# Kernel tuning notes

Measured on AMD Instinct MI355X. Metric: run time of the kernel, lower is better.

The kernel has to match this reference:

```python
import jax, jax.numpy as jnp
import numpy as np

EPS = 0.05
THRESH = 1e-6
MAX_ITER = 100


def _l2norm(x):
    # matches torch F.normalize(dim=-1): x / max(||x||, 1e-12)
    n = jnp.sqrt(jnp.sum(x * x, axis=-1, keepdims=True))
    return x / jnp.maximum(n, 1e-12)


def setup_inputs() -> dict:
    key = jax.random.key(0)
    kq, kk, kv = jax.random.split(key, 3)
    B, N, D = 8, 1024, 64
    return {
        "q": jax.random.normal(kq, (B, N, D), dtype=jnp.float32),
        "k": jax.random.normal(kk, (B, N, D), dtype=jnp.float32),
        "V": jax.random.normal(kv, (B, N, D), dtype=jnp.float32),
    }


def reference(q, k, V):
    B, N, D = q.shape
    Q = _l2norm(q)
    Kn = _l2norm(k)
    # cost matrix: 1 - cosine similarity, shape (B, N, N)
    C = 1.0 - jnp.einsum("bnd,bmd->bnm", Q, Kn)

    log_mu = jnp.full((B, N), jnp.log(1.0 / N + 1e-8), dtype=C.dtype)
    log_nu = log_mu

    def kernel(u, v):
        # (-C + u_i + v_j) / eps, shape (B, N, N)
        return (-C + u[:, :, None] + v[:, None, :]) / EPS

    def step(carry, _):
        u, v, done = carry
        u0 = u
        u_new = EPS * (log_mu - jax.scipy.special.logsumexp(kernel(u, v), axis=2)) + u
        v_new = EPS * (log_nu - jax.scipy.special.logsumexp(kernel(u_new, v), axis=1)) + v
        err = jnp.mean(jnp.abs(u_new - u0))
        # replicate torch early-break: once converged, freeze u, v
        u = jnp.where(done, u, u_new)
        v = jnp.where(done, v, v_new)
        done = jnp.logical_or(done, err < THRESH)
        return (u, v, done), None

    u0 = jnp.zeros((B, N), dtype=C.dtype)
    v0 = jnp.zeros((B, N), dtype=C.dtype)
    (u, v, _), _ = jax.lax.scan(
        jax.checkpoint(step), (u0, v0, jnp.array(False)), None, length=MAX_ITER
    )

    T = jnp.exp(kernel(u, v))  # transport plan (B, N, N)
    out = jnp.einsum("bnm,bmd->bnd", T, V) + V
    return out
```

## Files before the change

### kernel.cpp

```cpp
#include <hip/hip_runtime.h>
#include <math.h>

#define BB 8
#define NN 1024
#define DD 64
#define EPSF 0.05f
#define MAX_ITER 100
#define ERR_FX_THRESH 8590u
#define SCALE_ 28.853900817779268f
#define EPSLN2_ 0.034657359027997264f
#define NBLK 256
#define NPER 32

typedef __attribute__((ext_vector_type(8))) short short8;
typedef __attribute__((ext_vector_type(4))) float f32x4;

static __device__ __forceinline__ float fexp2(float x) { return __builtin_amdgcn_exp2f(x); }
static __device__ __forceinline__ float flog2(float x) { return __builtin_amdgcn_logf(x); }
static __device__ __forceinline__ float bflo(unsigned u) { return __uint_as_float(u << 16); }
static __device__ __forceinline__ unsigned short bf16rne(float x) {
    unsigned u = __float_as_uint(x);
    u += 0x7fffu + ((u >> 16) & 1u);
    return (unsigned short)(u >> 16);
}
__device__ __forceinline__ float wave_sum64(float x) {
#pragma unroll
    for (int off = 1; off < 64; off <<= 1) x += __shfl_xor(x, off);
    return x;
}

#define CNT64IDX(p, b) ((b) * 200 + (p))

__global__ __launch_bounds__(256) void norm_kernel(const float* __restrict__ q,
                                                   const float* __restrict__ k,
                                                   unsigned short* __restrict__ Qn,
                                                   unsigned short* __restrict__ Kn) {
    int tid = threadIdx.x;
    int bi = blockIdx.x;
    const float* src = (bi < 128) ? q : k;
    unsigned short* dst = (bi < 128) ? Qn : Kn;
    int row = (bi & 127) * 64 + (tid >> 2);
    int c = tid & 3;
    const float* rp = src + ((size_t)row << 6) + c * 16;
    float4 x0 = ((const float4*)rp)[0];
    float4 x1 = ((const float4*)rp)[1];
    float4 x2 = ((const float4*)rp)[2];
    float4 x3 = ((const float4*)rp)[3];
    float ss = x0.x * x0.x + x0.y * x0.y + x0.z * x0.z + x0.w * x0.w
             + x1.x * x1.x + x1.y * x1.y + x1.z * x1.z + x1.w * x1.w
             + x2.x * x2.x + x2.y * x2.y + x2.z * x2.z + x2.w * x2.w
             + x3.x * x3.x + x3.y * x3.y + x3.z * x3.z + x3.w * x3.w;
    ss += __shfl_xor(ss, 1);
    ss += __shfl_xor(ss, 2);
    float sc = 1.0f / fmaxf(sqrtf(ss), 1e-12f);
    unsigned pk[8];
    pk[0] = (unsigned)bf16rne(x0.x * sc) | ((unsigned)bf16rne(x0.y * sc) << 16);
    pk[1] = (unsigned)bf16rne(x0.z * sc) | ((unsigned)bf16rne(x0.w * sc) << 16);
    pk[2] = (unsigned)bf16rne(x1.x * sc) | ((unsigned)bf16rne(x1.y * sc) << 16);
    pk[3] = (unsigned)bf16rne(x1.z * sc) | ((unsigned)bf16rne(x1.w * sc) << 16);
    pk[4] = (unsigned)bf16rne(x2.x * sc) | ((unsigned)bf16rne(x2.y * sc) << 16);
    pk[5] = (unsigned)bf16rne(x2.z * sc) | ((unsigned)bf16rne(x2.w * sc) << 16);
    pk[6] = (unsigned)bf16rne(x3.x * sc) | ((unsigned)bf16rne(x3.y * sc) << 16);
    pk[7] = (unsigned)bf16rne(x3.z * sc) | ((unsigned)bf16rne(x3.w * sc) << 16);
    unsigned short* op = dst + ((size_t)row << 6) + c * 16;
    ((uint4*)op)[0] = make_uint4(pk[0], pk[1], pk[2], pk[3]);
    ((uint4*)op)[1] = make_uint4(pk[4], pk[5], pk[6], pk[7]);
}

__global__ __launch_bounds__(256) void cost_kernel(const unsigned short* __restrict__ Qn,
                                                   const unsigned short* __restrict__ Kn,
                                                   unsigned short* __restrict__ M,
                                                   unsigned short* __restrict__ MT,
                                                   float* __restrict__ vz) {
    __shared__ __align__(16) unsigned short Qb[64][72];
    __shared__ __align__(16) unsigned short Kb[64][72];
    __shared__ __align__(16) unsigned short Ms[64][72];
    __shared__ __align__(16) unsigned short MsT[64][72];
    int b = blockIdx.z;
    int i0 = blockIdx.y * 64, j0 = blockIdx.x * 64;
    int tid = threadIdx.x;
    if (blockIdx.x == 0 && blockIdx.y == 0 && blockIdx.z == 0) {
        float4 z4 = {0.f, 0.f, 0.f, 0.f};
        for (int i = tid; i < 2848; i += 256) ((float4*)vz)[i] = z4;
    }
#pragma unroll
    for (int s = 0; s < 2; ++s) {
        int idx = tid + 256 * s;
        int row = idx >> 3, seg = idx & 7;
        *(uint4*)&Qb[row][seg * 8] =
            *(const uint4*)(Qn + (((size_t)b * NN + i0 + row) << 6) + seg * 8);
        *(uint4*)&Kb[row][seg * 8] =
            *(const uint4*)(Kn + (((size_t)b * NN + j0 + row) << 6) + seg * 8);
    }
    __syncthreads();
    int w = tid >> 6, lane = tid & 63;
    int m = lane & 15, qq = lane >> 4;
    int rloc = w * 16;
    short8 a0 = *(const short8*)&Qb[rloc + m][qq * 8];
    short8 a1 = *(const short8*)&Qb[rloc + m][qq * 8 + 32];
    f32x4 acc[4];
#pragma unroll
    for (int nt = 0; nt < 4; ++nt) {
        short8 b0 = *(const short8*)&Kb[nt * 16 + m][qq * 8];
        short8 b1 = *(const short8*)&Kb[nt * 16 + m][qq * 8 + 32];
        f32x4 z = {0.f, 0.f, 0.f, 0.f};
        z = __builtin_amdgcn_mfma_f32_16x16x32_bf16(a0, b0, z, 0, 0, 0);
        acc[nt] = __builtin_amdgcn_mfma_f32_16x16x32_bf16(a1, b1, z, 0, 0, 0);
    }
#pragma unroll
    for (int nt = 0; nt < 4; ++nt) {
        unsigned short us[4];
#pragma unroll
        for (int r = 0; r < 4; ++r)
            us[r] = bf16rne(fexp2((acc[nt][r] - 1.0f) * SCALE_));
#pragma unroll
        for (int r = 0; r < 4; ++r)
            Ms[rloc + qq * 4 + r][nt * 16 + m] = us[r];
        uint2 t;
        t.x = (unsigned)us[0] | ((unsigned)us[1] << 16);
        t.y = (unsigned)us[2] | ((unsigned)us[3] << 16);
        *(uint2*)&MsT[nt * 16 + m][rloc + qq * 4] = t;
    }
    __syncthreads();
#pragma unroll
    for (int s = 0; s < 2; ++s) {
        int idx = tid + 256 * s;
        int row = idx >> 3, seg = idx & 7;
        *(uint4*)(M + ((size_t)b << 20) + ((size_t)(i0 + row) << 10) + j0 + seg * 8) =
            *(const uint4*)&Ms[row][seg * 8];
        *(uint4*)(MT + ((size_t)b << 20) + ((size_t)(j0 + row) << 10) + i0 + seg * 8) =
            *(const uint4*)&MsT[row][seg * 8];
    }
}

#define ACC8(U4, base)                                              \
    s0 = fmaf(bflo(U4.x), wrg[base + 0], s0);                       \
    s1 = fmaf(__uint_as_float(U4.x), wrg[base + 1], s1);            \
    s0 = fmaf(bflo(U4.y), wrg[base + 2], s0);                       \
    s1 = fmaf(__uint_as_float(U4.y), wrg[base + 3], s1);            \
    s0 = fmaf(bflo(U4.z), wrg[base + 4], s0);                       \
    s1 = fmaf(__uint_as_float(U4.z), wrg[base + 5], s1);            \
    s0 = fmaf(bflo(U4.w), wrg[base + 6], s0);                       \
    s1 = fmaf(__uint_as_float(U4.w), wrg[base + 7], s1);

__global__ __launch_bounds__(256, 1) void sink_coop(const unsigned short* __restrict__ M,
                                                    const unsigned short* MT,
                                                    float* __restrict__ u,
                                                    float* __restrict__ v,
                                                    unsigned long long* __restrict__ cnt64,
                                                    const float* __restrict__ V,
                                                    unsigned short* WT,
                                                    float eln) {
    __shared__ __align__(16) float sw[1280];
    __shared__ float sdel[4];
    __shared__ int sflag;
    int tid = threadIdx.x;
    int w = tid >> 6, lane = tid & 63;
    int b = blockIdx.x & 7;
    int slice = blockIdx.x >> 3;
    int rbase = slice * 32 + w * 8;
    const unsigned short* Mb  = M  + ((size_t)b << 20);
    const unsigned short* MTb = MT + ((size_t)b << 20);
    float* ub = u + (b << 10);
    float* vb = v + (b << 10);

    uint4 mA[8], mB[8], nA[8], nB[8];
#pragma unroll
    for (int r = 0; r < 8; ++r) {
        const uint4* rp = (const uint4*)(Mb + ((size_t)(rbase + r) << 10));
        mA[r] = rp[lane * 2];
        mB[r] = rp[lane * 2 + 1];
        const uint4* tp = (const uint4*)(MTb + ((size_t)(rbase + r) << 10));
        nA[r] = tp[lane * 2];
        nB[r] = tp[lane * 2 + 1];
    }

    float uprev[8], vreg[8];
#pragma unroll
    for (int r = 0; r < 8; ++r) { uprev[r] = 0.f; vreg[r] = 0.f; }

    unsigned myerr = 0xffffffffu;

    for (int t = 0; t < MAX_ITER; ++t) {
        {
            float4 ex;
            ex.x = fexp2(__hip_atomic_load(vb + tid * 4 + 0, __ATOMIC_RELAXED, __HIP_MEMORY_SCOPE_AGENT) * SCALE_);
            ex.y = fexp2(__hip_atomic_load(vb + tid * 4 + 1, __ATOMIC_RELAXED, __HIP_MEMORY_SCOPE_AGENT) * SCALE_);
            ex.z = fexp2(__hip_atomic_load(vb + tid * 4 + 2, __ATOMIC_RELAXED, __HIP_MEMORY_SCOPE_AGENT) * SCALE_);
            ex.w = fexp2(__hip_atomic_load(vb + tid * 4 + 3, __ATOMIC_RELAXED, __HIP_MEMORY_SCOPE_AGENT) * SCALE_);
            *(float4*)&sw[tid * 4 + 4 * (tid >> 2)] = ex;
            __syncthreads();
            float wrg[16];
            *(float4*)&wrg[0]  = *(const float4*)&sw[lane * 20 + 0];
            *(float4*)&wrg[4]  = *(const float4*)&sw[lane * 20 + 4];
            *(float4*)&wrg[8]  = *(const float4*)&sw[lane * 20 + 8];
            *(float4*)&wrg[12] = *(const float4*)&sw[lane * 20 + 12];
            float del = 0.f;
#pragma unroll
            for (int rr = 0; rr < 8; ++rr) {
                float s0 = 0.f, s1 = 0.f;
                ACC8(mA[rr], 0)
                ACC8(mB[rr], 8)
                float s = wave_sum64(s0 + s1);
                float un = eln - EPSLN2_ * flog2(s);
                del += fabsf(un - uprev[rr]);
                uprev[rr] = un;
                if (lane == 0)
                    __hip_atomic_store(ub + rbase + rr, un, __ATOMIC_RELAXED, __HIP_MEMORY_SCOPE_AGENT);
            }
            if (lane == 0) sdel[w] = del;
            asm volatile("s_waitcnt vmcnt(0)" ::: "memory");
            __syncthreads();
            if (tid == 0) {
                float dsum = sdel[0] + sdel[1] + sdel[2] + sdel[3];
                unsigned dfx = (unsigned)fminf(dsum * 1048576.0f, 6.0e7f) + 1u;
                unsigned long long* c = cnt64 + CNT64IDX(2 * t, b);
                unsigned long long tot =
                    __hip_atomic_fetch_add(c, (1ULL << 32) | (unsigned long long)dfx,
                                           __ATOMIC_RELAXED, __HIP_MEMORY_SCOPE_AGENT) +
                    ((1ULL << 32) | (unsigned long long)dfx);
                while ((unsigned)(tot >> 32) < NPER) {
                    __builtin_amdgcn_s_sleep(1);
                    tot = __hip_atomic_load(c, __ATOMIC_RELAXED, __HIP_MEMORY_SCOPE_AGENT);
                }
                myerr = (unsigned)tot;
            }
            __syncthreads();
        }
        {
            float4 ex;
            ex.x = fexp2(__hip_atomic_load(ub + tid * 4 + 0, __ATOMIC_RELAXED, __HIP_MEMORY_SCOPE_AGENT) * SCALE_);
            ex.y = fexp2(__hip_atomic_load(ub + tid * 4 + 1, __ATOMIC_RELAXED, __HIP_MEMORY_SCOPE_AGENT) * SCALE_);
            ex.z = fexp2(__hip_atomic_load(ub + tid * 4 + 2, __ATOMIC_RELAXED, __HIP_MEMORY_SCOPE_AGENT) * SCALE_);
            ex.w = fexp2(__hip_atomic_load(ub + tid * 4 + 3, __ATOMIC_RELAXED, __HIP_MEMORY_SCOPE_AGENT) * SCALE_);
            *(float4*)&sw[tid * 4 + 4 * (tid >> 2)] = ex;
            __syncthreads();
            float wrg[16];
            *(float4*)&wrg[0]  = *(const float4*)&sw[lane * 20 + 0];
            *(float4*)&wrg[4]  = *(const float4*)&sw[lane * 20 + 4];
            *(float4*)&wrg[8]  = *(const float4*)&sw[lane * 20 + 8];
            *(float4*)&wrg[12] = *(const float4*)&sw[lane * 20 + 12];
#pragma unroll
            for (int rr = 0; rr < 8; ++rr) {
                float s0 = 0.f, s1 = 0.f;
                ACC8(nA[rr], 0)
                ACC8(nB[rr], 8)
                float s = wave_sum64(s0 + s1);
                float vn = eln - EPSLN2_ * flog2(s);
                vreg[rr] = vn;
                if (lane == 0)
                    __hip_atomic_store(vb + rbase + rr, vn, __ATOMIC_RELAXED, __HIP_MEMORY_SCOPE_AGENT);
            }
            asm volatile("s_waitcnt vmcnt(0)" ::: "memory");
            __syncthreads();
            if (tid == 0) {
                unsigned long long* c = cnt64 + CNT64IDX(2 * t + 1, b);
                unsigned long long tot =
                    __hip_atomic_fetch_add(c, 1ULL << 32, __ATOMIC_RELAXED, __HIP_MEMORY_SCOPE_AGENT) +
                    (1ULL << 32);
                while ((unsigned)(tot >> 32) < NPER) {
                    __builtin_amdgcn_s_sleep(1);
                    tot = __hip_atomic_load(c, __ATOMIC_RELAXED, __HIP_MEMORY_SCOPE_AGENT);
                }
                int brk = 0;
                if (myerr < ERR_FX_THRESH) {
                    unsigned long long s = 0;
                    for (int bb = 0; bb < 8; ++bb) {
                        unsigned long long tv = __hip_atomic_load(cnt64 + CNT64IDX(2 * t, bb),
                                                                  __ATOMIC_RELAXED, __HIP_MEMORY_SCOPE_AGENT);
                        while ((unsigned)(tv >> 32) < NPER) {
                            __builtin_amdgcn_s_sleep(1);
                            tv = __hip_atomic_load(cnt64 + CNT64IDX(2 * t, bb),
                                                   __ATOMIC_RELAXED, __HIP_MEMORY_SCOPE_AGENT);
                        }
                        s += (unsigned long long)(unsigned)tv;
                    }
                    brk = (s < (unsigned long long)ERR_FX_THRESH);
                }
                sflag = brk;
            }
            __syncthreads();
            if (sflag) break;
        }
    }

    {
        __syncthreads();
        float* swj = &sw[1152];
        unsigned short* T = (unsigned short*)sw;
#pragma unroll
        for (int r = 0; r < 8; ++r)
            if (lane == r) swj[w * 8 + r] = fexp2(vreg[r] * SCALE_);
        __syncthreads();
        int jr = lane >> 3;
        int seg = lane & 7;
        int j = rbase + jr;
        float wj = swj[w * 8 + jr];
        const float* Vp = V + ((((size_t)(b << 10)) + j) << 6) + seg * 8;
        float4 x0 = *(const float4*)(Vp);
        float4 x1 = *(const float4*)(Vp + 4);
        int jloc = w * 8 + jr;
        int d0 = seg * 8;
        T[(d0 + 0) * 36 + jloc] = bf16rne(x0.x * wj);
        T[(d0 + 1) * 36 + jloc] = bf16rne(x0.y * wj);
        T[(d0 + 2) * 36 + jloc] = bf16rne(x0.z * wj);
        T[(d0 + 3) * 36 + jloc] = bf16rne(x0.w * wj);
        T[(d0 + 4) * 36 + jloc] = bf16rne(x1.x * wj);
        T[(d0 + 5) * 36 + jloc] = bf16rne(x1.y * wj);
        T[(d0 + 6) * 36 + jloc] = bf16rne(x1.z * wj);
        T[(d0 + 7) * 36 + jloc] = bf16rne(x1.w * wj);
        __syncthreads();
        int d = tid >> 2, q4 = tid & 3;
        const unsigned short* tr = &T[d * 36 + q4 * 8];
        uint4 o;
        o.x = (unsigned)tr[0] | ((unsigned)tr[1] << 16);
        o.y = (unsigned)tr[2] | ((unsigned)tr[3] << 16);
        o.z = (unsigned)tr[4] | ((unsigned)tr[5] << 16);
        o.w = (unsigned)tr[6] | ((unsigned)tr[7] << 16);
        *(uint4*)(WT + ((size_t)b << 16) + ((size_t)d << 10) + slice * 32 + q4 * 8) = o;
    }
}

__global__ __launch_bounds__(256) void gemm_final(const unsigned short* __restrict__ M,
                                                  const unsigned short* __restrict__ WT,
                                                  const float* __restrict__ u,
                                                  const float* __restrict__ V,
                                                  float* __restrict__ out) {
    __shared__ float sa[32];
    int tid = threadIdx.x;
    int w = tid >> 6, lane = tid & 63;
    int b = blockIdx.x & 7, mt = blockIdx.x >> 3;
    if (tid < 32) sa[tid] = fexp2(u[(b << 10) + mt * 32 + tid] * SCALE_);
    __syncthreads();
    int m = lane & 15, q = lane >> 4;
    int rloc = (w & 1) * 16;
    int nbase = (w >> 1) * 32;
    const unsigned short* Ma = M + ((size_t)b << 20) + ((size_t)(mt * 32 + rloc + m) << 10) + q * 8;
    const unsigned short* W0 = WT + ((size_t)b << 16) + ((size_t)(nbase + m) << 10) + q * 8;
    const unsigned short* W1 = W0 + (16 << 10);
    f32x4 acc0 = {0.f, 0.f, 0.f, 0.f}, acc1 = {0.f, 0.f, 0.f, 0.f};
#pragma unroll 4
    for (int k0 = 0; k0 < NN; k0 += 32) {
        short8 af = *(const short8*)(Ma + k0);
        short8 b0 = *(const short8*)(W0 + k0);
        short8 b1 = *(const short8*)(W1 + k0);
        acc0 = __builtin_amdgcn_mfma_f32_16x16x32_bf16(af, b0, acc0, 0, 0, 0);
        acc1 = __builtin_amdgcn_mfma_f32_16x16x32_bf16(af, b1, acc1, 0, 0, 0);
    }
#pragma unroll
    for (int r = 0; r < 4; ++r) {
        int lrow = rloc + q * 4 + r;
        int gm = mt * 32 + lrow;
        float a = sa[lrow];
        size_t base = (((size_t)b << 10) + gm) * DD;
        int n0 = nbase + m;
        out[base + n0]      = fmaf(a, acc0[r], V[base + n0]);
        out[base + n0 + 16] = fmaf(a, acc1[r], V[base + n0 + 16]);
    }
}

extern "C" void kernel_launch(void* const* d_in, const int* in_sizes, int n_in,
                              void* d_out, int out_size, void* d_ws, size_t ws_size,
                              hipStream_t stream) {
    const float* q = (const float*)d_in[0];
    const float* k = (const float*)d_in[1];
    const float* V = (const float*)d_in[2];
    float* out = (float*)d_out;

    char* ws = (char*)d_ws;
    const size_t MB16 = (size_t)BB * NN * NN * sizeof(unsigned short);
    unsigned short* M  = (unsigned short*)ws;
    unsigned short* MT = (unsigned short*)(ws + MB16);
    unsigned short* WT = MT;
    float* u   = (float*)(ws + 2 * MB16);
    float* v   = u + BB * NN;
    unsigned long long* cnt64 = (unsigned long long*)(v + BB * NN);

    unsigned short* Qn = (unsigned short*)out;
    unsigned short* Kn = Qn + (size_t)BB * NN * DD;

    norm_kernel<<<256, 256, 0, stream>>>(q, k, Qn, Kn);

    cost_kernel<<<dim3(16, 16, 8), 256, 0, stream>>>(Qn, Kn, M, MT, v);

    float eln = EPSF * logf(1.0f / NN + 1e-8f);
    sink_coop<<<dim3(NBLK), dim3(256), 0, stream>>>(M, MT, u, v, cnt64, V, WT, eln);

    gemm_final<<<256, 256, 0, stream>>>(M, WT, u, V, out);
}
```

Measured before the change: 176.6 us.

## Fuse final transport-plan GEMM into cooperative Sinkhorn kernel using register-resident M

```diff
diff --git a/kernel.cpp b/kernel.cpp
--- a/kernel.cpp
+++ b/kernel.cpp
@@ -11,6 +11,7 @@
 #define EPSLN2_ 0.034657359027997264f
 #define NBLK 256
 #define NPER 32
+#define MPITCH 1032
 
 typedef __attribute__((ext_vector_type(8))) short short8;
 typedef __attribute__((ext_vector_type(4))) float f32x4;
@@ -144,16 +145,21 @@
     s1 = fmaf(__uint_as_float(U4.w), wrg[base + 7], s1);
 
 __global__ __launch_bounds__(256, 1) void sink_coop(const unsigned short* __restrict__ M,
-                                                    const unsigned short* MT,
+                                                    const unsigned short* __restrict__ MT,
                                                     float* __restrict__ u,
                                                     float* __restrict__ v,
                                                     unsigned long long* __restrict__ cnt64,
                                                     const float* __restrict__ V,
-                                                    unsigned short* WT,
+                                                    float* __restrict__ out,
                                                     float eln) {
     __shared__ __align__(16) float sw[1280];
     __shared__ float sdel[4];
     __shared__ int sflag;
+    __shared__ __align__(16) unsigned short Mslab[32 * MPITCH];
+    __shared__ __align__(16) float Vs[64][65];
+    __shared__ __align__(16) unsigned short WTl[64 * 72];
+    __shared__ float wjL[1024];
+    __shared__ float sa[32];
     int tid = threadIdx.x;
     int w = tid >> 6, lane = tid & 63;
     int b = blockIdx.x & 7;
@@ -175,9 +181,9 @@
         nB[r] = tp[lane * 2 + 1];
     }
 
-    float uprev[8], vreg[8];
-#pragma unroll
-    for (int r = 0; r < 8; ++r) { uprev[r] = 0.f; vreg[r] = 0.f; }
+    float uprev[8];
+#pragma unroll
+    for (int r = 0; r < 8; ++r) uprev[r] = 0.f;
 
     unsigned myerr = 0xffffffffu;
 
@@ -247,7 +253,6 @@
                 ACC8(nB[rr], 8)
                 float s = wave_sum64(s0 + s1);
                 float vn = eln - EPSLN2_ * flog2(s);
-                vreg[rr] = vn;
                 if (lane == 0)
                     __hip_atomic_store(vb + rbase + rr, vn, __ATOMIC_RELAXED, __HIP_MEMORY_SCOPE_AGENT);
             }
@@ -285,77 +290,76 @@
     }
 
     {
-        __syncthreads();
-        float* swj = &sw[1152];
-        unsigned short* T = (unsigned short*)sw;
+        {
+            float a0 = __hip_atomic_load(vb + tid * 4 + 0, __ATOMIC_RELAXED, __HIP_MEMORY_SCOPE_AGENT);
+            float a1 = __hip_atomic_load(vb + tid * 4 + 1, __ATOMIC_RELAXED, __HIP_MEMORY_SCOPE_AGENT);
+            float a2 = __hip_atomic_load(vb + tid * 4 + 2, __ATOMIC_RELAXED, __HIP_MEMORY_SCOPE_AGENT);
+            float a3 = __hip_atomic_load(vb + tid * 4 + 3, __ATOMIC_RELAXED, __HIP_MEMORY_SCOPE_AGENT);
+            wjL[tid * 4 + 0] = fexp2(a0 * SCALE_);
+            wjL[tid * 4 + 1] = fexp2(a1 * SCALE_);
+            wjL[tid * 4 + 2] = fexp2(a2 * SCALE_);
+            wjL[tid * 4 + 3] = fexp2(a3 * SCALE_);
+        }
 #pragma unroll
         for (int r = 0; r < 8; ++r)
-            if (lane == r) swj[w * 8 + r] = fexp2(vreg[r] * SCALE_);
-        __syncthreads();
-        int jr = lane >> 3;
-        int seg = lane & 7;
-        int j = rbase + jr;
-        float wj = swj[w * 8 + jr];
-        const float* Vp = V + ((((size_t)(b << 10)) + j) << 6) + seg * 8;
-        float4 x0 = *(const float4*)(Vp);
-        float4 x1 = *(const float4*)(Vp + 4);
-        int jloc = w * 8 + jr;
-        int d0 = seg * 8;
-        T[(d0 + 0) * 36 + jloc] = bf16rne(x0.x * wj);
-        T[(d0 + 1) * 36 + jloc] = bf16rne(x0.y * wj);
-        T[(d0 + 2) * 36 + jloc] = bf16rne(x0.z * wj);
-        T[(d0 + 3) * 36 + jloc] = bf16rne(x0.w * wj);
-        T[(d0 + 4) * 36 + jloc] = bf16rne(x1.x * wj);
-        T[(d0 + 5) * 36 + jloc] = bf16rne(x1.y * wj);
-        T[(d0 + 6) * 36 + jloc] = bf16rne(x1.z * wj);
-        T[(d0 + 7) * 36 + jloc] = bf16rne(x1.w * wj);
-        __syncthreads();
-        int d = tid >> 2, q4 = tid & 3;
-        const unsigned short* tr = &T[d * 36 + q4 * 8];
-        uint4 o;
-        o.x = (unsigned)tr[0] | ((unsigned)tr[1] << 16);
-        o.y = (unsigned)tr[2] | ((unsigned)tr[3] << 16);
-        o.z = (unsigned)tr[4] | ((unsigned)tr[5] << 16);
-        o.w = (unsigned)tr[6] | ((unsigned)tr[7] << 16);
-        *(uint4*)(WT + ((size_t)b << 16) + ((size_t)d << 10) + slice * 32 + q4 * 8) = o;
-    }
-}
-
-__global__ __launch_bounds__(256) void gemm_final(const unsigned short* __restrict__ M,
-                                                  const unsigned short* __restrict__ WT,
-                                                  const float* __restrict__ u,
-                                                  const float* __restrict__ V,
-                                                  float* __restrict__ out) {
-    __shared__ float sa[32];
-    int tid = threadIdx.x;
-    int w = tid >> 6, lane = tid & 63;
-    int b = blockIdx.x & 7, mt = blockIdx.x >> 3;
-    if (tid < 32) sa[tid] = fexp2(u[(b << 10) + mt * 32 + tid] * SCALE_);
-    __syncthreads();
-    int m = lane & 15, q = lane >> 4;
-    int rloc = (w & 1) * 16;
-    int nbase = (w >> 1) * 32;
-    const unsigned short* Ma = M + ((size_t)b << 20) + ((size_t)(mt * 32 + rloc + m) << 10) + q * 8;
-    const unsigned short* W0 = WT + ((size_t)b << 16) + ((size_t)(nbase + m) << 10) + q * 8;
-    const unsigned short* W1 = W0 + (16 << 10);
-    f32x4 acc0 = {0.f, 0.f, 0.f, 0.f}, acc1 = {0.f, 0.f, 0.f, 0.f};
-#pragma unroll 4
-    for (int k0 = 0; k0 < NN; k0 += 32) {
-        short8 af = *(const short8*)(Ma + k0);
-        short8 b0 = *(const short8*)(W0 + k0);
-        short8 b1 = *(const short8*)(W1 + k0);
-        acc0 = __builtin_amdgcn_mfma_f32_16x16x32_bf16(af, b0, acc0, 0, 0, 0);
-        acc1 = __builtin_amdgcn_mfma_f32_16x16x32_bf16(af, b1, acc1, 0, 0, 0);
-    }
-#pragma unroll
-    for (int r = 0; r < 4; ++r) {
-        int lrow = rloc + q * 4 + r;
-        int gm = mt * 32 + lrow;
-        float a = sa[lrow];
-        size_t base = (((size_t)b << 10) + gm) * DD;
-        int n0 = nbase + m;
-        out[base + n0]      = fmaf(a, acc0[r], V[base + n0]);
-        out[base + n0 + 16] = fmaf(a, acc1[r], V[base + n0 + 16]);
+            if (lane == r) sa[w * 8 + r] = fexp2(uprev[r] * SCALE_);
+#pragma unroll
+        for (int r = 0; r < 8; ++r) {
+            int row = w * 8 + r;
+            *(uint4*)&Mslab[row * MPITCH + lane * 16]     = mA[r];
+            *(uint4*)&Mslab[row * MPITCH + lane * 16 + 8] = mB[r];
+        }
+        int m2 = lane & 15, q2 = lane >> 4;
+        int rloc2 = (w & 1) * 16;
+        int nbase2 = (w >> 1) * 32;
+        f32x4 acc0 = {0.f, 0.f, 0.f, 0.f}, acc1 = {0.f, 0.f, 0.f, 0.f};
+        const float* Vb2 = V + ((size_t)b << 16);
+        for (int jc = 0; jc < 16; ++jc) {
+#pragma unroll
+            for (int c = 0; c < 4; ++c) {
+                int idx = tid + 256 * c;
+                int row = idx >> 4, c4 = idx & 15;
+                float4 x = ((const float4*)(Vb2 + ((size_t)(jc * 64 + row) << 6)))[c4];
+                Vs[row][c4 * 4 + 0] = x.x; Vs[row][c4 * 4 + 1] = x.y;
+                Vs[row][c4 * 4 + 2] = x.z; Vs[row][c4 * 4 + 3] = x.w;
+            }
+            __syncthreads();
+            {
+                int d = tid >> 2, qd = tid & 3;
+                unsigned pk[8];
+#pragma unroll
+                for (int p = 0; p < 8; ++p) {
+                    int j = qd * 16 + p * 2;
+                    unsigned lo = bf16rne(Vs[j][d] * wjL[jc * 64 + j]);
+                    unsigned hi = bf16rne(Vs[j + 1][d] * wjL[jc * 64 + j + 1]);
+                    pk[p] = lo | (hi << 16);
+                }
+                unsigned short* dst = &WTl[d * 72 + qd * 16];
+                ((uint4*)dst)[0] = make_uint4(pk[0], pk[1], pk[2], pk[3]);
+                ((uint4*)dst)[1] = make_uint4(pk[4], pk[5], pk[6], pk[7]);
+            }
+            __syncthreads();
+            short8 a0 = *(const short8*)&Mslab[(rloc2 + m2) * MPITCH + jc * 64 + q2 * 8];
+            short8 a1 = *(const short8*)&Mslab[(rloc2 + m2) * MPITCH + jc * 64 + q2 * 8 + 32];
+            short8 b00 = *(const short8*)&WTl[(nbase2 + m2) * 72 + q2 * 8];
+            short8 b01 = *(const short8*)&WTl[(nbase2 + m2) * 72 + q2 * 8 + 32];
+            short8 b10 = *(const short8*)&WTl[(nbase2 + m2 + 16) * 72 + q2 * 8];
+            short8 b11 = *(const short8*)&WTl[(nbase2 + m2 + 16) * 72 + q2 * 8 + 32];
+            acc0 = __builtin_amdgcn_mfma_f32_16x16x32_bf16(a0, b00, acc0, 0, 0, 0);
+            acc1 = __builtin_amdgcn_mfma_f32_16x16x32_bf16(a0, b10, acc1, 0, 0, 0);
+            acc0 = __builtin_amdgcn_mfma_f32_16x16x32_bf16(a1, b01, acc0, 0, 0, 0);
+            acc1 = __builtin_amdgcn_mfma_f32_16x16x32_bf16(a1, b11, acc1, 0, 0, 0);
+        }
+#pragma unroll
+        for (int r = 0; r < 4; ++r) {
+            int lrow = rloc2 + q2 * 4 + r;
+            int gm = slice * 32 + lrow;
+            float a = sa[lrow];
+            size_t base = (((size_t)b << 10) + gm) * DD;
+            int n0 = nbase2 + m2;
+            out[base + n0]      = fmaf(a, acc0[r], V[base + n0]);
+            out[base + n0 + 16] = fmaf(a, acc1[r], V[base + n0 + 16]);
+        }
     }
 }
 
@@ -371,7 +375,6 @@
     const size_t MB16 = (size_t)BB * NN * NN * sizeof(unsigned short);
     unsigned short* M  = (unsigned short*)ws;
     unsigned short* MT = (unsigned short*)(ws + MB16);
-    unsigned short* WT = MT;
     float* u   = (float*)(ws + 2 * MB16);
     float* v   = u + BB * NN;
     unsigned long long* cnt64 = (unsigned long long*)(v + BB * NN);
@@ -384,7 +387,5 @@
     cost_kernel<<<dim3(16, 16, 8), 256, 0, stream>>>(Qn, Kn, M, MT, v);
 
     float eln = EPSF * logf(1.0f / NN + 1e-8f);
-    sink_coop<<<dim3(NBLK), dim3(256), 0, stream>>>(M, MT, u, v, cnt64, V, WT, eln);
-
-    gemm_final<<<256, 256, 0, stream>>>(M, WT, u, V, out);
-}
+    sink_coop<<<dim3(NBLK), dim3(256), 0, stream>>>(M, MT, u, v, cnt64, V, out, eln);
+}
```

Result: no change. 179.4 us (+1.6%).
